# Optimization experiments

Measured on AMD Instinct MI355X. Metric: run time of the kernel, lower is better.

## Reference

```python
import jax, jax.numpy as jnp
import numpy as np

B, S, D = 2, 2048, 2048
H = 32
HD = D // H  # 64
EPS = 1e-4


def setup_inputs() -> dict:
    key = jax.random.key(0)
    ks = jax.random.split(key, 9)
    hidden_states = jax.random.normal(ks[0], (B, S, D), dtype=jnp.float32)
    # multiplicative causal mask
    attention_mask = jnp.tril(jnp.ones((S, S), dtype=jnp.float32))[None, None]
    scale = 0.02
    wq = jax.random.normal(ks[1], (D, D), dtype=jnp.float32) * scale
    wk = jax.random.normal(ks[2], (D, D), dtype=jnp.float32) * scale
    wv = jax.random.normal(ks[3], (D, D), dtype=jnp.float32) * scale
    wo = jax.random.normal(ks[4], (D, D), dtype=jnp.float32) * scale
    bq = jax.random.normal(ks[5], (D,), dtype=jnp.float32) * scale
    bk = jax.random.normal(ks[6], (D,), dtype=jnp.float32) * scale
    bv = jax.random.normal(ks[7], (D,), dtype=jnp.float32) * scale
    bo = jax.random.normal(ks[8], (D,), dtype=jnp.float32) * scale
    return {"hidden_states": hidden_states, "attention_mask": attention_mask,
            "wq": wq, "bq": bq, "wk": wk, "bk": bk, "wv": wv, "bv": bv,
            "wo": wo, "bo": bo}


def _split_heads(x):
    # [B, S, D] -> [B, H, S, HD]
    b, s, _ = x.shape
    return x.reshape(b, s, H, HD).transpose(0, 2, 1, 3)


def reference(hidden_states, attention_mask, wq, bq, wk, bk, wv, bv, wo, bo):
    scaling = HD ** -0.5
    q = (hidden_states @ wq.T + bq) * scaling
    k = hidden_states @ wk.T + bk
    v = hidden_states @ wv.T + bv
    q, k, v = _split_heads(q), _split_heads(k), _split_heads(v)
    # ELU+1 feature map, then sum-normalize over head dim
    q = jax.nn.elu(q) + 1.0
    k = jax.nn.elu(k) + 1.0
    q = q / (q.sum(-1, keepdims=True) + EPS)
    k = k / (k.sum(-1, keepdims=True) + EPS)
    # quadratic attention: [B, H, S, S]
    attn = jnp.einsum('bhsd,bhtd->bhst', q, k) * (HD ** -0.5)
    attn = attn * attention_mask  # multiplicative mask
    out = jnp.einsum('bhst,bhtd->bhsd', attn, v)  # [B, H, S, HD]
    out = out.transpose(0, 2, 1, 3).reshape(hidden_states.shape[0], -1, D)
    return out @ wo.T + bo
```

## Files before the change

kernel.cpp:

```cpp
#include <hip/hip_runtime.h>

typedef __bf16 bf16x8 __attribute__((ext_vector_type(8)));
typedef float f32x4 __attribute__((ext_vector_type(4)));

#define GLDS(g, l) __builtin_amdgcn_global_load_lds(                              \
    (const __attribute__((address_space(1))) void*)(g),                            \
    (__attribute__((address_space(3))) void*)(l), 16, 0, 0)

__device__ __forceinline__ unsigned short f2bf(float f) {
  unsigned int u = __builtin_bit_cast(unsigned int, f);
  u = (u + 0x7fffu + ((u >> 16) & 1u)) >> 16;
  return (unsigned short)u;
}
__device__ __forceinline__ float bf2f(unsigned short h) {
  unsigned int u = ((unsigned int)h) << 16;
  return __builtin_bit_cast(float, u);
}

__global__ __launch_bounds__(256) void cvt_f32_bf16(
    const float* __restrict__ in, unsigned short* __restrict__ out, int n4) {
  int i = blockIdx.x * 256 + threadIdx.x;
  if (i < n4) {
    float4 v = ((const float4*)in)[i];
    ushort4 o;
    o.x = f2bf(v.x); o.y = f2bf(v.y); o.z = f2bf(v.z); o.w = f2bf(v.w);
    ((ushort4*)out)[i] = o;
  }
}

template<int MODE, int NB, int CX, int CY>
__global__ __launch_bounds__(512, 2) void gemm128(
    const unsigned short* __restrict__ A, const unsigned short* __restrict__ Bw,
    const float* __restrict__ b0, const float* __restrict__ b1, const float* __restrict__ b2,
    void* __restrict__ o0, void* __restrict__ o1, void* __restrict__ o2) {
  constexpr int K = 2048, NT = 32;
  __shared__ unsigned short lds[73728];
  const int tid = threadIdx.x, lane = tid & 63, wid = tid >> 6;
  const int wm = wid >> 2, wn = wid & 3;

  constexpr int NWG = (NB / 256) * 32;
  constexpr int CPX = NWG >> 3;
  constexpr int CCOLS = (NB / 256) / CX;
  const int g0 = blockIdx.x;
  const int wg = (g0 & 7) * CPX + (g0 >> 3);
  const int l = wg % (CX * CY);
  const int chunk = wg / (CX * CY);
  const int bx = (chunk % CCOLS) * CX + l / CY;
  const int by = (chunk / CCOLS) * CY + l % CY;

  const int rloc = wid * 8 + (lane >> 3);
  const size_t gcoff = (size_t)(((lane & 7) ^ (lane >> 3)) << 3);
  const unsigned short* gA[2];
  const unsigned short* gB[4];
#pragma unroll
  for (int c = 0; c < 2; ++c) gA[c] = A + (size_t)(by * 128 + c * 64 + rloc) * K + gcoff;
#pragma unroll
  for (int c = 0; c < 4; ++c) gB[c] = Bw + (size_t)(bx * 256 + c * 64 + rloc) * K + gcoff;

  int aoff[4][2], boff[4][2];
#pragma unroll
  for (int m = 0; m < 4; ++m)
#pragma unroll
    for (int kk = 0; kk < 2; ++kk) {
      aoff[m][kk] = (wm * 64 + m * 16 + (lane & 15)) * 64 +
                    ((((kk << 2) + (lane >> 4)) ^ (lane & 7)) << 3);
      boff[m][kk] = (wn * 64 + m * 16 + (lane & 15)) * 64 +
                    ((((kk << 2) + (lane >> 4)) ^ (lane & 7)) << 3);
    }

  f32x4 acc[4][4] = {};

#define AB(b) ((b) * 8192)
#define BB(b) (24576 + (b) * 16384)
#define STAGE_A(c, b) GLDS(gA[c], lds + AB(b) + (c) * 4096 + wid * 512)
#define STAGE_B(c, b) GLDS(gB[c], lds + BB(b) + (c) * 4096 + wid * 512)

  STAGE_A(0, 0); STAGE_A(1, 0); STAGE_B(0, 0); STAGE_B(1, 0); STAGE_B(2, 0); STAGE_B(3, 0);
#pragma unroll
  for (int c = 0; c < 2; ++c) gA[c] += 64;
#pragma unroll
  for (int c = 0; c < 4; ++c) gB[c] += 64;
  STAGE_A(0, 1); STAGE_A(1, 1); STAGE_B(0, 1); STAGE_B(1, 1); STAGE_B(2, 1); STAGE_B(3, 1);
#pragma unroll
  for (int c = 0; c < 2; ++c) gA[c] += 64;
#pragma unroll
  for (int c = 0; c < 4; ++c) gB[c] += 64;
  asm volatile("s_waitcnt vmcnt(6)" ::: "memory");
  __builtin_amdgcn_s_barrier();

  for (int t = 0; t < NT; ++t) {
    const int b = t % 3;
    const int sb = (t + 2) % 3;
    const bool doStage = (t + 2 < NT);

    if (doStage) { STAGE_A(0, sb); STAGE_A(1, sb); STAGE_B(0, sb); STAGE_B(1, sb); }
    bf16x8 af[4], bfr[4];
#pragma unroll
    for (int m = 0; m < 4; ++m) af[m] = *(const bf16x8*)&lds[AB(b) + aoff[m][0]];
#pragma unroll
    for (int n = 0; n < 4; ++n) bfr[n] = *(const bf16x8*)&lds[BB(b) + boff[n][0]];
    __builtin_amdgcn_s_barrier();
    __builtin_amdgcn_s_setprio(1);
#pragma unroll
    for (int m = 0; m < 4; ++m)
#pragma unroll
      for (int n = 0; n < 4; ++n)
        acc[m][n] = __builtin_amdgcn_mfma_f32_16x16x32_bf16(af[m], bfr[n], acc[m][n], 0, 0, 0);
    __builtin_amdgcn_s_setprio(0);
    __builtin_amdgcn_s_barrier();

    if (doStage) { STAGE_B(2, sb); STAGE_B(3, sb); }
#pragma unroll
    for (int c = 0; c < 2; ++c) gA[c] += 64;
#pragma unroll
    for (int c = 0; c < 4; ++c) gB[c] += 64;
#pragma unroll
    for (int m = 0; m < 4; ++m) af[m] = *(const bf16x8*)&lds[AB(b) + aoff[m][1]];
#pragma unroll
    for (int n = 0; n < 4; ++n) bfr[n] = *(const bf16x8*)&lds[BB(b) + boff[n][1]];
    __builtin_amdgcn_s_barrier();
    __builtin_amdgcn_s_setprio(1);
#pragma unroll
    for (int m = 0; m < 4; ++m)
#pragma unroll
      for (int n = 0; n < 4; ++n)
        acc[m][n] = __builtin_amdgcn_mfma_f32_16x16x32_bf16(af[m], bfr[n], acc[m][n], 0, 0, 0);
    __builtin_amdgcn_s_setprio(0);
    if (t < NT - 1) {
      if (doStage) asm volatile("s_waitcnt vmcnt(6)" ::: "memory");
      else         asm volatile("s_waitcnt vmcnt(0)" ::: "memory");
    }
    __builtin_amdgcn_s_barrier();
  }

  if constexpr (MODE == 0) {
    float* C = (float*)o0;
#pragma unroll
    for (int n = 0; n < 4; ++n) {
      const int col = bx * 256 + wn * 64 + n * 16 + (lane & 15);
      const float bv_ = b0[col];
#pragma unroll
      for (int m = 0; m < 4; ++m) {
        const int row0 = by * 128 + wm * 64 + m * 16 + ((lane >> 4) << 2);
#pragma unroll
        for (int r = 0; r < 4; ++r)
          C[(size_t)(row0 + r) * 2048 + col] = acc[m][n][r] + bv_;
      }
    }
  } else {
    const int head = bx * 4 + wn;
    const int type = head >> 5;
    const int h = head & 31;
    const float* bias = (type == 0) ? b0 : (type == 1) ? b1 : b2;
    unsigned short* dst = (unsigned short*)((type == 0) ? o0 : (type == 1) ? o1 : o2);
    float bvals[4];
#pragma unroll
    for (int n = 0; n < 4; ++n) bvals[n] = bias[h * 64 + n * 16 + (lane & 15)];
#pragma unroll
    for (int m = 0; m < 4; ++m) {
#pragma unroll
      for (int r = 0; r < 4; ++r) {
        const int row = by * 128 + wm * 64 + m * 16 + ((lane >> 4) << 2) + r;
        const int bb = row >> 11, s = row & 2047;
        float e[4];
        float loc = 0.f;
#pragma unroll
        for (int n = 0; n < 4; ++n) {
          float v = acc[m][n][r] + bvals[n];
          if (type == 0) v *= 0.125f;
          if (type < 2) v = (v > 0.f) ? (v + 1.f) : __expf(v);
          e[n] = v; loc += v;
        }
        if (type < 2) {
#pragma unroll
          for (int off = 1; off < 16; off <<= 1) loc += __shfl_xor(loc, off, 64);
          const float inv = 1.f / (loc + 1e-4f);
#pragma unroll
          for (int n = 0; n < 4; ++n) e[n] *= inv;
        }
        const size_t base = ((size_t)((bb << 5) + h) * 2048 + s) * 64;
#pragma unroll
        for (int n = 0; n < 4; ++n) dst[base + n * 16 + (lane & 15)] = f2bf(e[n]);
      }
    }
  }
#undef AB
#undef BB
#undef STAGE_A
#undef STAGE_B
}

__global__ __launch_bounds__(256) void chunk_state(
    const unsigned short* __restrict__ Kn, const unsigned short* __restrict__ Vn,
    unsigned short* __restrict__ stT) {
  __shared__ unsigned short Kt[64 * 72];
  __shared__ unsigned short Vt[64 * 72];
  const int c = blockIdx.x, bh = blockIdx.y;
  const int tid = threadIdx.x, lane = tid & 63, wid = tid >> 6;
  const size_t base = (size_t)bh * 2048 * 64 + (size_t)c * 64 * 64;
#pragma unroll
  for (int i = 0; i < 16; ++i) {
    const int ii = i * 256 + tid;
    const int t = ii >> 6, d = ii & 63;
    Kt[d * 72 + t] = Kn[base + ii];
    Vt[d * 72 + t] = Vn[base + ii];
  }
  __syncthreads();
  f32x4 acc[4] = {};
#pragma unroll
  for (int ks = 0; ks < 2; ++ks) {
    const int ko = ks * 32 + (lane >> 4) * 8;
    bf16x8 a = *(const bf16x8*)&Vt[(wid * 16 + (lane & 15)) * 72 + ko];
#pragma unroll
    for (int ej = 0; ej < 4; ++ej) {
      bf16x8 bb = *(const bf16x8*)&Kt[(ej * 16 + (lane & 15)) * 72 + ko];
      acc[ej] = __builtin_amdgcn_mfma_f32_16x16x32_bf16(a, bb, acc[ej], 0, 0, 0);
    }
  }
  const size_t obase = ((size_t)bh * 32 + c) * 4096;
#pragma unroll
  for (int ej = 0; ej < 4; ++ej) {
    const int e = ej * 16 + (lane & 15);
    const int d0 = wid * 16 + ((lane >> 4) << 2);
#pragma unroll
    for (int r = 0; r < 4; ++r)
      stT[obase + (size_t)(d0 + r) * 64 + e] = f2bf(acc[ej][r]);
  }
}

__global__ __launch_bounds__(256) void prefix_state(
    const unsigned short* __restrict__ stT, unsigned short* __restrict__ cumT) {
  const int g = blockIdx.x * 256 + threadIdx.x;
  const int bh = g >> 12, e = g & 4095;
  float run = 0.f;
  for (int c = 0; c < 32; ++c) {
    const size_t idx = (((size_t)bh * 32 + c) << 12) + e;
    const float v = bf2f(stT[idx]);
    cumT[idx] = f2bf(run);
    run += v;
  }
}

__global__ __launch_bounds__(256) void attn_intra(
    const unsigned short* __restrict__ Qn, const unsigned short* __restrict__ Kn,
    const unsigned short* __restrict__ Vn, const unsigned short* __restrict__ cumT,
    unsigned short* __restrict__ aout) {
  __shared__ unsigned short Qs[64 * 72];
  __shared__ unsigned short Ks[64 * 72];
  __shared__ unsigned short Vt[64 * 72];
  __shared__ unsigned short St[64 * 72];
  __shared__ unsigned short Ps[64 * 72];
  const int c = blockIdx.x, bh = blockIdx.y;
  const int tid = threadIdx.x, lane = tid & 63, wid = tid >> 6;
  const size_t base = (size_t)bh * 2048 * 64 + (size_t)c * 64 * 64;
  const size_t sbase = ((size_t)bh * 32 + c) * 4096;
#pragma unroll
  for (int i = 0; i < 16; ++i) {
    const int ii = i * 256 + tid;
    const int t = ii >> 6, d = ii & 63;
    Qs[t * 72 + d] = Qn[base + ii];
    Ks[t * 72 + d] = Kn[base + ii];
    Vt[d * 72 + t] = Vn[base + ii];
    St[t * 72 + d] = cumT[sbase + ii];
  }
  __syncthreads();
  f32x4 sacc[4] = {};
#pragma unroll
  for (int ks = 0; ks < 2; ++ks) {
    const int ko = ks * 32 + (lane >> 4) * 8;
    bf16x8 a = *(const bf16x8*)&Qs[(wid * 16 + (lane & 15)) * 72 + ko];
#pragma unroll
    for (int tj = 0; tj < 4; ++tj) {
      bf16x8 bb = *(const bf16x8*)&Ks[(tj * 16 + (lane & 15)) * 72 + ko];
      sacc[tj] = __builtin_amdgcn_mfma_f32_16x16x32_bf16(a, bb, sacc[tj], 0, 0, 0);
    }
  }
#pragma unroll
  for (int tj = 0; tj < 4; ++tj) {
    const int t = tj * 16 + (lane & 15);
    const int s0 = wid * 16 + ((lane >> 4) << 2);
#pragma unroll
    for (int r = 0; r < 4; ++r) {
      const float v = (t <= s0 + r) ? sacc[tj][r] : 0.f;
      Ps[(s0 + r) * 72 + t] = f2bf(v);
    }
  }
  __syncthreads();
  f32x4 oacc[4] = {};
#pragma unroll
  for (int ks = 0; ks < 2; ++ks) {
    const int ko = ks * 32 + (lane >> 4) * 8;
    bf16x8 a = *(const bf16x8*)&Ps[(wid * 16 + (lane & 15)) * 72 + ko];
    bf16x8 a2 = *(const bf16x8*)&Qs[(wid * 16 + (lane & 15)) * 72 + ko];
#pragma unroll
    for (int dj = 0; dj < 4; ++dj) {
      bf16x8 bv_ = *(const bf16x8*)&Vt[(dj * 16 + (lane & 15)) * 72 + ko];
      oacc[dj] = __builtin_amdgcn_mfma_f32_16x16x32_bf16(a, bv_, oacc[dj], 0, 0, 0);
      bf16x8 bs_ = *(const bf16x8*)&St[(dj * 16 + (lane & 15)) * 72 + ko];
      oacc[dj] = __builtin_amdgcn_mfma_f32_16x16x32_bf16(a2, bs_, oacc[dj], 0, 0, 0);
    }
  }
  const int b = bh >> 5, h = bh & 31;
#pragma unroll
  for (int dj = 0; dj < 4; ++dj) {
    const int d = dj * 16 + (lane & 15);
    const int s0 = wid * 16 + ((lane >> 4) << 2);
#pragma unroll
    for (int r = 0; r < 4; ++r) {
      const size_t row = (size_t)(b * 2048 + c * 64 + s0 + r);
      aout[row * 2048 + h * 64 + d] = f2bf(0.125f * oacc[dj][r]);
    }
  }
}

extern "C" void kernel_launch(void* const* d_in, const int* in_sizes, int n_in,
                              void* d_out, int out_size, void* d_ws, size_t ws_size,
                              hipStream_t stream) {
  const float* hs = (const float*)d_in[0];
  const float* wq = (const float*)d_in[2];
  const float* bq = (const float*)d_in[3];
  const float* wk = (const float*)d_in[4];
  const float* bk = (const float*)d_in[5];
  const float* wv = (const float*)d_in[6];
  const float* bv = (const float*)d_in[7];
  const float* wo = (const float*)d_in[8];
  const float* bo = (const float*)d_in[9];
  float* out = (float*)d_out;
  char* ws = (char*)d_ws;

  unsigned short* hs_bf   = (unsigned short*)(ws);
  unsigned short* wqkv_bf = (unsigned short*)(ws + 16777216);
  unsigned short* wo_bf   = (unsigned short*)(ws + 41943040);
  unsigned short* Qn      = (unsigned short*)(ws + 50331648);
  unsigned short* Kn      = (unsigned short*)(ws + 67108864);
  unsigned short* Vn      = (unsigned short*)(ws + 83886080);
  unsigned short* stT     = (unsigned short*)(ws + 100663296);
  unsigned short* cumT    = (unsigned short*)(ws + 117440512);
  unsigned short* aout    = (unsigned short*)(ws + 134217728);

  cvt_f32_bf16<<<8192, 256, 0, stream>>>(hs, hs_bf, 2097152);
  cvt_f32_bf16<<<4096, 256, 0, stream>>>(wq, wqkv_bf, 1048576);
  cvt_f32_bf16<<<4096, 256, 0, stream>>>(wk, wqkv_bf + 4194304, 1048576);
  cvt_f32_bf16<<<4096, 256, 0, stream>>>(wv, wqkv_bf + 8388608, 1048576);
  cvt_f32_bf16<<<4096, 256, 0, stream>>>(wo, wo_bf, 1048576);

  gemm128<1, 6144, 6, 16><<<768, 512, 0, stream>>>(
      hs_bf, wqkv_bf, bq, bk, bv, Qn, Kn, Vn);

  chunk_state<<<dim3(32, 64), 256, 0, stream>>>(Kn, Vn, stT);
  prefix_state<<<1024, 256, 0, stream>>>(stT, cumT);
  attn_intra<<<dim3(32, 64), 256, 0, stream>>>(Qn, Kn, Vn, cumT, aout);

  gemm128<0, 2048, 2, 16><<<256, 512, 0, stream>>>(
      aout, wo_bf, bo, nullptr, nullptr, out, nullptr, nullptr);
}
```

Baseline: 218.3 us.

## Use 256x256 tiles for QKV GEMM and merge weight conversions into one launch

```diff
diff --git a/kernel.cpp b/kernel.cpp
--- a/kernel.cpp
+++ b/kernel.cpp
@@ -28,34 +28,214 @@
   }
 }
 
-template<int MODE, int NB, int CX, int CY>
-__global__ __launch_bounds__(512, 2) void gemm128(
+__global__ __launch_bounds__(256) void cvt_w4(
+    const float* __restrict__ w0, const float* __restrict__ w1,
+    const float* __restrict__ w2, const float* __restrict__ w3,
+    unsigned short* __restrict__ out) {
+  const int y = blockIdx.y;
+  const float* src = (y == 0) ? w0 : (y == 1) ? w1 : (y == 2) ? w2 : w3;
+  const int i = blockIdx.x * 256 + threadIdx.x;
+  float4 v = ((const float4*)src)[i];
+  ushort4 o;
+  o.x = f2bf(v.x); o.y = f2bf(v.y); o.z = f2bf(v.z); o.w = f2bf(v.w);
+  ((ushort4*)(out + (size_t)y * 4194304))[i] = o;
+}
+
+__global__ __launch_bounds__(512, 2) void gemm256_qkv(
     const unsigned short* __restrict__ A, const unsigned short* __restrict__ Bw,
-    const float* __restrict__ b0, const float* __restrict__ b1, const float* __restrict__ b2,
-    void* __restrict__ o0, void* __restrict__ o1, void* __restrict__ o2) {
+    const float* __restrict__ bq, const float* __restrict__ bk, const float* __restrict__ bv,
+    unsigned short* __restrict__ oQ, unsigned short* __restrict__ oK,
+    unsigned short* __restrict__ oV) {
+  constexpr int K = 2048, NT = 32;
+  __shared__ unsigned short lds[81920];
+  const int tid = threadIdx.x, lane = tid & 63, wid = tid >> 6;
+  const int wm = wid >> 2, wn = wid & 3;
+
+  const int g0 = blockIdx.x;
+  const int wg = (g0 & 7) * 48 + (g0 >> 3);
+  const int l = wg % 96, chunk = wg / 96;
+  const int bx = chunk * 6 + l / 16;
+  const int by = l % 16;
+
+  const int rloc = tid >> 3;
+  const size_t gcoff = (size_t)(((lane & 7) ^ (lane >> 3)) << 3);
+  const unsigned short* gA[4];
+  const unsigned short* gB[4];
+#pragma unroll
+  for (int c = 0; c < 4; ++c) {
+    gA[c] = A  + (size_t)(by * 256 + c * 64 + rloc) * K + gcoff;
+    gB[c] = Bw + (size_t)(bx * 256 + c * 64 + rloc) * K + gcoff;
+  }
+
+#define ABu(b) ((b) * 16384)
+#define BBu(b) (49152 + (b) * 16384)
+#define STAGE_A(c, b) GLDS(gA[c], lds + ABu(b) + (c) * 4096 + wid * 512)
+#define STAGE_B(c, b) GLDS(gB[c], lds + BBu(b) + (c) * 4096 + wid * 512)
+
+  const int arow = (wm * 128 + (lane & 15)) * 64;
+  const int brow = (wn * 64 + (lane & 15)) * 64;
+  const int sw0 = (((lane >> 4)) ^ (lane & 7)) << 3;
+  const int sw1 = ((4 + (lane >> 4)) ^ (lane & 7)) << 3;
+
+  f32x4 acc[8][4] = {};
+
+#pragma unroll
+  for (int c = 0; c < 4; ++c) STAGE_A(c, 0);
+#pragma unroll
+  for (int c = 0; c < 4; ++c) gA[c] += 64;
+#pragma unroll
+  for (int c = 0; c < 4; ++c) STAGE_B(c, 0);
+#pragma unroll
+  for (int c = 0; c < 4; ++c) gB[c] += 64;
+#pragma unroll
+  for (int c = 0; c < 4; ++c) STAGE_A(c, 1);
+#pragma unroll
+  for (int c = 0; c < 4; ++c) gA[c] += 64;
+  asm volatile("s_waitcnt vmcnt(4)" ::: "memory");
+  __builtin_amdgcn_s_barrier();
+
+  for (int t = 0; t < NT; ++t) {
+    const int Ab = ABu(t % 3) + arow;
+    const int Bb = BBu(t & 1) + brow;
+    const int Asb = (t + 2) % 3, Bsb = (t + 1) & 1;
+    const bool stA = (t + 2 < NT), stB = (t + 1 < NT);
+    bf16x8 Af[4], Bf[4];
+
+    if (stB) { STAGE_B(0, Bsb); STAGE_B(1, Bsb); }
+#pragma unroll
+    for (int n = 0; n < 4; ++n) Bf[n] = *(const bf16x8*)&lds[Bb + n * 1024 + sw0];
+#pragma unroll
+    for (int m = 0; m < 4; ++m) Af[m] = *(const bf16x8*)&lds[Ab + m * 1024 + sw0];
+    __builtin_amdgcn_s_barrier();
+    __builtin_amdgcn_s_setprio(1);
+#pragma unroll
+    for (int m = 0; m < 4; ++m)
+#pragma unroll
+      for (int n = 0; n < 4; ++n)
+        acc[m][n] = __builtin_amdgcn_mfma_f32_16x16x32_bf16(Af[m], Bf[n], acc[m][n], 0, 0, 0);
+    __builtin_amdgcn_s_setprio(0);
+    __builtin_amdgcn_s_barrier();
+
+    if (stB) {
+      STAGE_B(2, Bsb); STAGE_B(3, Bsb);
+#pragma unroll
+      for (int c = 0; c < 4; ++c) gB[c] += 64;
+    }
+#pragma unroll
+    for (int m = 0; m < 4; ++m) Af[m] = *(const bf16x8*)&lds[Ab + (m + 4) * 1024 + sw0];
+    __builtin_amdgcn_s_barrier();
+    __builtin_amdgcn_s_setprio(1);
+#pragma unroll
+    for (int m = 0; m < 4; ++m)
+#pragma unroll
+      for (int n = 0; n < 4; ++n)
+        acc[m + 4][n] = __builtin_amdgcn_mfma_f32_16x16x32_bf16(Af[m], Bf[n], acc[m + 4][n], 0, 0, 0);
+    __builtin_amdgcn_s_setprio(0);
+    __builtin_amdgcn_s_barrier();
+
+    if (stA) { STAGE_A(0, Asb); STAGE_A(1, Asb); }
+#pragma unroll
+    for (int n = 0; n < 4; ++n) Bf[n] = *(const bf16x8*)&lds[Bb + n * 1024 + sw1];
+#pragma unroll
+    for (int m = 0; m < 4; ++m) Af[m] = *(const bf16x8*)&lds[Ab + m * 1024 + sw1];
+    __builtin_amdgcn_s_barrier();
+    __builtin_amdgcn_s_setprio(1);
+#pragma unroll
+    for (int m = 0; m < 4; ++m)
+#pragma unroll
+      for (int n = 0; n < 4; ++n)
+        acc[m][n] = __builtin_amdgcn_mfma_f32_16x16x32_bf16(Af[m], Bf[n], acc[m][n], 0, 0, 0);
+    __builtin_amdgcn_s_setprio(0);
+    __builtin_amdgcn_s_barrier();
+
+    if (stA) {
+      STAGE_A(2, Asb); STAGE_A(3, Asb);
+#pragma unroll
+      for (int c = 0; c < 4; ++c) gA[c] += 64;
+    }
+#pragma unroll
+    for (int m = 0; m < 4; ++m) Af[m] = *(const bf16x8*)&lds[Ab + (m + 4) * 1024 + sw1];
+    __builtin_amdgcn_s_barrier();
+    __builtin_amdgcn_s_setprio(1);
+#pragma unroll
+    for (int m = 0; m < 4; ++m)
+#pragma unroll
+      for (int n = 0; n < 4; ++n)
+        acc[m + 4][n] = __builtin_amdgcn_mfma_f32_16x16x32_bf16(Af[m], Bf[n], acc[m + 4][n], 0, 0, 0);
+    __builtin_amdgcn_s_setprio(0);
+    if (stA)      asm volatile("s_waitcnt vmcnt(4)" ::: "memory");
+    else if (stB) asm volatile("s_waitcnt vmcnt(0)" ::: "memory");
+    __builtin_amdgcn_s_barrier();
+  }
+
+  const int head = bx * 4 + wn;
+  const int type = head >> 5;
+  const int h = head & 31;
+  const float* bias = (type == 0) ? bq : (type == 1) ? bk : bv;
+  unsigned short* dst = (type == 0) ? oQ : (type == 1) ? oK : oV;
+  float bv4[4];
+#pragma unroll
+  for (int n = 0; n < 4; ++n) bv4[n] = bias[h * 64 + n * 16 + (lane & 15)];
+#pragma unroll
+  for (int m = 0; m < 8; ++m) {
+#pragma unroll
+    for (int r = 0; r < 4; ++r) {
+      const int row = by * 256 + wm * 128 + m * 16 + ((lane >> 4) << 2) + r;
+      const int bb = row >> 11, s = row & 2047;
+      float e[4];
+      float loc = 0.f;
+#pragma unroll
+      for (int n = 0; n < 4; ++n) {
+        float v = acc[m][n][r] + bv4[n];
+        if (type == 0) v *= 0.125f;
+        if (type < 2) v = (v > 0.f) ? (v + 1.f) : __expf(v);
+        e[n] = v; loc += v;
+      }
+      if (type < 2) {
+#pragma unroll
+        for (int off = 1; off < 16; off <<= 1) loc += __shfl_xor(loc, off, 64);
+        const float inv = 1.f / (loc + 1e-4f);
+#pragma unroll
+        for (int n = 0; n < 4; ++n) e[n] *= inv;
+      }
+      const size_t base = ((size_t)((bb << 5) + h) * 2048 + s) * 64;
+#pragma unroll
+      for (int n = 0; n < 4; ++n) dst[base + n * 16 + (lane & 15)] = f2bf(e[n]);
+    }
+  }
+#undef ABu
+#undef BBu
+#undef STAGE_A
+#undef STAGE_B
+}
+
+__global__ __launch_bounds__(512, 2) void gemm128_wo(
+    const unsigned short* __restrict__ A, const unsigned short* __restrict__ Bw,
+    const float* __restrict__ b0, float* __restrict__ C) {
   constexpr int K = 2048, NT = 32;
   __shared__ unsigned short lds[73728];
   const int tid = threadIdx.x, lane = tid & 63, wid = tid >> 6;
   const int wm = wid >> 2, wn = wid & 3;
 
-  constexpr int NWG = (NB / 256) * 32;
-  constexpr int CPX = NWG >> 3;
-  constexpr int CCOLS = (NB / 256) / CX;
+  constexpr int NWG = 256, CPX = NWG >> 3;
   const int g0 = blockIdx.x;
   const int wg = (g0 & 7) * CPX + (g0 >> 3);
-  const int l = wg % (CX * CY);
-  const int chunk = wg / (CX * CY);
-  const int bx = (chunk % CCOLS) * CX + l / CY;
-  const int by = (chunk / CCOLS) * CY + l % CY;
+  const int l = wg % 32;
+  const int chunk = wg / 32;
+  const int bx = chunk * 2 + l / 16;
+  const int by = l % 16 + ((chunk >= 4) ? 0 : 0);
+  const int bx2 = (chunk % 4) * 2 + l / 16;
+  const int by2 = (chunk / 4) * 16 + l % 16;
+  (void)bx; (void)by;
 
   const int rloc = wid * 8 + (lane >> 3);
   const size_t gcoff = (size_t)(((lane & 7) ^ (lane >> 3)) << 3);
   const unsigned short* gA[2];
   const unsigned short* gB[4];
 #pragma unroll
-  for (int c = 0; c < 2; ++c) gA[c] = A + (size_t)(by * 128 + c * 64 + rloc) * K + gcoff;
-#pragma unroll
-  for (int c = 0; c < 4; ++c) gB[c] = Bw + (size_t)(bx * 256 + c * 64 + rloc) * K + gcoff;
+  for (int c = 0; c < 2; ++c) gA[c] = A + (size_t)(by2 * 128 + c * 64 + rloc) * K + gcoff;
+#pragma unroll
+  for (int c = 0; c < 4; ++c) gB[c] = Bw + (size_t)(bx2 * 256 + c * 64 + rloc) * K + gcoff;
 
   int aoff[4][2], boff[4][2];
 #pragma unroll
@@ -133,55 +313,16 @@
     __builtin_amdgcn_s_barrier();
   }
 
-  if constexpr (MODE == 0) {
-    float* C = (float*)o0;
-#pragma unroll
-    for (int n = 0; n < 4; ++n) {
-      const int col = bx * 256 + wn * 64 + n * 16 + (lane & 15);
-      const float bv_ = b0[col];
-#pragma unroll
-      for (int m = 0; m < 4; ++m) {
-        const int row0 = by * 128 + wm * 64 + m * 16 + ((lane >> 4) << 2);
-#pragma unroll
-        for (int r = 0; r < 4; ++r)
-          C[(size_t)(row0 + r) * 2048 + col] = acc[m][n][r] + bv_;
-      }
-    }
-  } else {
-    const int head = bx * 4 + wn;
-    const int type = head >> 5;
-    const int h = head & 31;
-    const float* bias = (type == 0) ? b0 : (type == 1) ? b1 : b2;
-    unsigned short* dst = (unsigned short*)((type == 0) ? o0 : (type == 1) ? o1 : o2);
-    float bvals[4];
-#pragma unroll
-    for (int n = 0; n < 4; ++n) bvals[n] = bias[h * 64 + n * 16 + (lane & 15)];
+#pragma unroll
+  for (int n = 0; n < 4; ++n) {
+    const int col = bx2 * 256 + wn * 64 + n * 16 + (lane & 15);
+    const float bv_ = b0[col];
 #pragma unroll
     for (int m = 0; m < 4; ++m) {
-#pragma unroll
-      for (int r = 0; r < 4; ++r) {
-        const int row = by * 128 + wm * 64 + m * 16 + ((lane >> 4) << 2) + r;
-        const int bb = row >> 11, s = row & 2047;
-        float e[4];
-        float loc = 0.f;
-#pragma unroll
-        for (int n = 0; n < 4; ++n) {
-          float v = acc[m][n][r] + bvals[n];
-          if (type == 0) v *= 0.125f;
-          if (type < 2) v = (v > 0.f) ? (v + 1.f) : __expf(v);
-          e[n] = v; loc += v;
-        }
-        if (type < 2) {
-#pragma unroll
-          for (int off = 1; off < 16; off <<= 1) loc += __shfl_xor(loc, off, 64);
-          const float inv = 1.f / (loc + 1e-4f);
-#pragma unroll
-          for (int n = 0; n < 4; ++n) e[n] *= inv;
-        }
-        const size_t base = ((size_t)((bb << 5) + h) * 2048 + s) * 64;
-#pragma unroll
-        for (int n = 0; n < 4; ++n) dst[base + n * 16 + (lane & 15)] = f2bf(e[n]);
-      }
+      const int row0 = by2 * 128 + wm * 64 + m * 16 + ((lane >> 4) << 2);
+#pragma unroll
+      for (int r = 0; r < 4; ++r)
+        C[(size_t)(row0 + r) * 2048 + col] = acc[m][n][r] + bv_;
     }
   }
 #undef AB
@@ -329,8 +470,7 @@
   char* ws = (char*)d_ws;
 
   unsigned short* hs_bf   = (unsigned short*)(ws);
-  unsigned short* wqkv_bf = (unsigned short*)(ws + 16777216);
-  unsigned short* wo_bf   = (unsigned short*)(ws + 41943040);
+  unsigned short* wall_bf = (unsigned short*)(ws + 16777216);
   unsigned short* Qn      = (unsigned short*)(ws + 50331648);
   unsigned short* Kn      = (unsigned short*)(ws + 67108864);
   unsigned short* Vn      = (unsigned short*)(ws + 83886080);
@@ -339,18 +479,13 @@
   unsigned short* aout    = (unsigned short*)(ws + 134217728);
 
   cvt_f32_bf16<<<8192, 256, 0, stream>>>(hs, hs_bf, 2097152);
-  cvt_f32_bf16<<<4096, 256, 0, stream>>>(wq, wqkv_bf, 1048576);
-  cvt_f32_bf16<<<4096, 256, 0, stream>>>(wk, wqkv_bf + 4194304, 1048576);
-  cvt_f32_bf16<<<4096, 256, 0, stream>>>(wv, wqkv_bf + 8388608, 1048576);
-  cvt_f32_bf16<<<4096, 256, 0, stream>>>(wo, wo_bf, 1048576);
-
-  gemm128<1, 6144, 6, 16><<<768, 512, 0, stream>>>(
-      hs_bf, wqkv_bf, bq, bk, bv, Qn, Kn, Vn);
+  cvt_w4<<<dim3(4096, 4), 256, 0, stream>>>(wq, wk, wv, wo, wall_bf);
+
+  gemm256_qkv<<<384, 512, 0, stream>>>(hs_bf, wall_bf, bq, bk, bv, Qn, Kn, Vn);
 
   chunk_state<<<dim3(32, 64), 256, 0, stream>>>(Kn, Vn, stT);
   prefix_state<<<1024, 256, 0, stream>>>(stT, cumT);
   attn_intra<<<dim3(32, 64), 256, 0, stream>>>(Qn, Kn, Vn, cumT, aout);
 
-  gemm128<0, 2048, 2, 16><<<256, 512, 0, stream>>>(
-      aout, wo_bf, bo, nullptr, nullptr, out, nullptr, nullptr);
-}
+  gemm128_wo<<<256, 512, 0, stream>>>(aout, wall_bf + 12582912, bo, out);
+}
```

After: 229.4 us. +5.1%, slower.
